# Performance work log

Hardware: AMD Instinct MI355X
Metric: run time of the kernel (lower is better)

Reference implementation:

```python
import jax, jax.numpy as jnp
import numpy as np
from jax import lax

B, T, D, U = 128, 1024, 256, 48


def setup_inputs() -> dict:
    key = jax.random.key(0)
    k1, k2, k3 = jax.random.split(key, 3)
    x = jax.random.normal(k1, (B, T, D), dtype=jnp.float32)
    kernel = jax.random.normal(k2, (D, U), dtype=jnp.float32) * (1.0 / np.sqrt(D))
    bias = jnp.zeros((U,), dtype=jnp.float32)
    chain_kernel = jax.random.normal(k3, (U, U), dtype=jnp.float32)
    return {"x": x, "kernel": kernel, "bias": bias, "chain_kernel": chain_kernel}


def _viterbi_decode(logits, trans):
    # logits: [B, T, U], trans: [U, U]; full-length sequences (mask=None)
    init_state = logits[:, 0]  # [B, U]
    steps = jnp.swapaxes(logits[:, 1:], 0, 1)  # [T-1, B, U]

    def fwd(state, logit_t):
        # scores[b, i, j] = state[b, i] + trans[i, j]
        scores = state[:, :, None] + trans[None]  # [B, U, U]
        bp = jnp.argmax(scores, axis=1)            # [B, U] best prev tag
        new_state = logit_t + jnp.max(scores, axis=1)
        return new_state, bp

    final_state, bps = lax.scan(fwd, init_state, steps)  # bps: [T-1, B, U]
    last_tag = jnp.argmax(final_state, axis=-1)          # [B]

    def back(tag, bp):
        prev = jnp.take_along_axis(bp, tag[:, None], axis=1)[:, 0]
        return prev, prev

    # reverse scan emits tags for t = 0..T-2 in forward time order
    _, tags_head = lax.scan(back, last_tag, bps, reverse=True)  # [T-1, B]
    tags = jnp.concatenate([tags_head, last_tag[None]], axis=0)  # [T, B]
    return jnp.transpose(tags)  # [B, T]


def reference(x, kernel, bias, chain_kernel):
    # _dense_layer: linear activation -> x @ kernel + bias
    logits = jnp.einsum('btd,du->btu', x, kernel) + bias  # [B, T, U]
    pred_ids = _viterbi_decode(logits, chain_kernel)       # [B, T] int
    return pred_ids.astype(jnp.float32)
```

## Files before the change

### kernel.cpp

```cpp
#include <hip/hip_runtime.h>
#include <cstdint>

#define B_ 128
#define T_ 1024
#define D_ 256
#define U_ 48

__global__ __launch_bounds__(256, 1) void k_logits(const float* __restrict__ x,
                                                   const float* __restrict__ kern,
                                                   const float* __restrict__ bias,
                                                   float* __restrict__ logits) {
    __shared__ float K[D_ * U_];
    __shared__ float bsh[U_];
    const int tid = threadIdx.x;
    for (int i = tid; i < D_ * U_; i += 256) K[i] = kern[i];
    if (tid < U_) bsh[tid] = bias[tid];
    __syncthreads();

    const long row0 = (long)blockIdx.x * 256 + tid;
    const long row1 = row0 + (long)B_ * T_ / 2;
    const float4* xr0 = (const float4*)(x + row0 * D_);
    const float4* xr1 = (const float4*)(x + row1 * D_);

    float a0[U_], a1[U_];
#pragma unroll
    for (int u = 0; u < U_; ++u) { a0[u] = 0.0f; a1[u] = 0.0f; }

#pragma unroll 1
    for (int d4 = 0; d4 < D_ / 4; ++d4) {
        const float4 xv0 = xr0[d4];
        const float4 xv1 = xr1[d4];
        const float xc0[4] = {xv0.x, xv0.y, xv0.z, xv0.w};
        const float xc1[4] = {xv1.x, xv1.y, xv1.z, xv1.w};
#pragma unroll
        for (int c = 0; c < 4; ++c) {
            const float4* kp = (const float4*)&K[(d4 * 4 + c) * U_];
            const float s0 = xc0[c], s1 = xc1[c];
#pragma unroll
            for (int u4 = 0; u4 < U_ / 4; ++u4) {
                float4 kv = kp[u4];
                a0[u4 * 4 + 0] += s0 * kv.x;  a1[u4 * 4 + 0] += s1 * kv.x;
                a0[u4 * 4 + 1] += s0 * kv.y;  a1[u4 * 4 + 1] += s1 * kv.y;
                a0[u4 * 4 + 2] += s0 * kv.z;  a1[u4 * 4 + 2] += s1 * kv.z;
                a0[u4 * 4 + 3] += s0 * kv.w;  a1[u4 * 4 + 3] += s1 * kv.w;
            }
        }
    }

    float4* o0 = (float4*)(logits + row0 * U_);
    float4* o1 = (float4*)(logits + row1 * U_);
#pragma unroll
    for (int i = 0; i < U_ / 4; ++i) {
        float4 v0, v1;
        v0.x = a0[i*4+0] + bsh[i*4+0];  v1.x = a1[i*4+0] + bsh[i*4+0];
        v0.y = a0[i*4+1] + bsh[i*4+1];  v1.y = a1[i*4+1] + bsh[i*4+1];
        v0.z = a0[i*4+2] + bsh[i*4+2];  v1.z = a1[i*4+2] + bsh[i*4+2];
        v0.w = a0[i*4+3] + bsh[i*4+3];  v1.w = a1[i*4+3] + bsh[i*4+3];
        o0[i] = v0;
        o1[i] = v1;
    }
}

__device__ __forceinline__ float step_max_lds(const float4* sb, const float* tc) {
    float n0 = -3.0e38f, n1 = -3.0e38f, n2 = -3.0e38f, n3 = -3.0e38f;
#pragma unroll
    for (int k = 0; k < U_ / 4; k += 4) {
        float4 s0 = sb[k + 0];
        float4 s1 = sb[k + 1];
        float4 s2 = sb[k + 2];
        float4 s3 = sb[k + 3];
        n0 = fmaxf(n0, fmaxf(fmaxf(s0.x + tc[4*k + 0],  s0.y + tc[4*k + 1]),
                             fmaxf(s0.z + tc[4*k + 2],  s0.w + tc[4*k + 3])));
        n1 = fmaxf(n1, fmaxf(fmaxf(s1.x + tc[4*k + 4],  s1.y + tc[4*k + 5]),
                             fmaxf(s1.z + tc[4*k + 6],  s1.w + tc[4*k + 7])));
        n2 = fmaxf(n2, fmaxf(fmaxf(s2.x + tc[4*k + 8],  s2.y + tc[4*k + 9]),
                             fmaxf(s2.z + tc[4*k + 10], s2.w + tc[4*k + 11])));
        n3 = fmaxf(n3, fmaxf(fmaxf(s3.x + tc[4*k + 12], s3.y + tc[4*k + 13]),
                             fmaxf(s3.z + tc[4*k + 14], s3.w + tc[4*k + 15])));
    }
    return fmaxf(fmaxf(n0, n1), fmaxf(n2, n3));
}

__global__ __launch_bounds__(64, 1) void k_forward(const float* __restrict__ trans,
                                                   const float* __restrict__ logits,
                                                   float* __restrict__ delta) {
    __shared__ float4 sbuf[2][U_ / 4];
    const int lane = threadIdx.x;
    const int b = blockIdx.x;
    const int u = (lane < U_) ? lane : (U_ - 1);

    float tc[U_];
#pragma unroll
    for (int v = 0; v < U_; ++v) tc[v] = trans[v * U_ + u];

    const float* lin = logits + (long)b * T_ * U_;
    float* dout = delta + (long)b * T_ * U_;

    float state = lin[u];
    dout[u] = state;
    ((float*)sbuf[0])[u] = state;

    float pf[8];
#pragma unroll
    for (int i = 0; i < 8; ++i) pf[i] = lin[(1 + i) * U_ + u];

    const float* lp = lin + 9 * U_ + u;
    float* dp = dout + 1 * U_ + u;

#pragma unroll 1
    for (int g = 0; g < 127; ++g) {
#pragma unroll
        for (int j = 0; j < 8; ++j) {
            const float logit = pf[j];
            pf[j] = lp[j * U_];

            const float4* sb = sbuf[j & 1];
            const float m = step_max_lds(sb, tc);
            state = logit + m;
            ((float*)sbuf[(j & 1) ^ 1])[u] = state;
            dp[j * U_] = state;
        }
        lp += 8 * U_;
        dp += 8 * U_;
    }

#pragma unroll
    for (int j = 0; j < 7; ++j) {
        const float logit = pf[j];
        const float4* sb = sbuf[j & 1];
        const float m = step_max_lds(sb, tc);
        state = logit + m;
        ((float*)sbuf[(j & 1) ^ 1])[u] = state;
        dp[j * U_] = state;
    }
}

__global__ __launch_bounds__(64, 1) void k_forward_inplace(const float* __restrict__ trans,
                                                           float* __restrict__ delta) {
    __shared__ float4 sbuf[2][U_ / 4];
    const int lane = threadIdx.x;
    const int b = blockIdx.x;
    const int u = (lane < U_) ? lane : (U_ - 1);

    float tc[U_];
#pragma unroll
    for (int v = 0; v < U_; ++v) tc[v] = trans[v * U_ + u];

    float* base = delta + (long)b * T_ * U_;
    float state = base[u];
    ((float*)sbuf[0])[u] = state;

#pragma unroll 1
    for (int t = 1; t < T_; ++t) {
        const float logit = base[(long)t * U_ + u];
        const float m = step_max_lds(sbuf[(t - 1) & 1], tc);
        state = logit + m;
        ((float*)sbuf[t & 1])[u] = state;
        base[(long)t * U_ + u] = state;
    }
}

__global__ __launch_bounds__(64, 1) void k_bp(const float* __restrict__ trans,
                                              const float* __restrict__ delta,
                                              unsigned char* __restrict__ bp) {
    const int lane = threadIdx.x;
    const int u = (lane < U_) ? lane : (U_ - 1);

    float tc[U_];
#pragma unroll
    for (int v = 0; v < U_; ++v) tc[v] = trans[v * U_ + u];

    const int NROW = B_ * (T_ - 1);
    const int stride = gridDim.x;

    int row = blockIdx.x;
    float dnext = 0.0f;
    if (row < NROW) {
        int b = row / (T_ - 1);
        int t = row - b * (T_ - 1) + 1;
        dnext = delta[((long)b * T_ + (t - 1)) * U_ + u];
    }
#pragma unroll 1
    for (; row < NROW; row += stride) {
        const float dv = dnext;
        const int rn = row + stride;
        if (rn < NROW) {
            int bn = rn / (T_ - 1);
            int tn = rn - bn * (T_ - 1) + 1;
            dnext = delta[((long)bn * T_ + (tn - 1)) * U_ + u];
        }
        const int db = __float_as_int(dv);
        float best = -3.4e38f;
        int bi = 0;
#pragma unroll
        for (int v = 0; v < U_; ++v) {
            float c = __int_as_float(__builtin_amdgcn_readlane(db, v)) + tc[v];
            if (c > best) { best = c; bi = v; }
        }
        if (lane < U_) bp[(long)row * U_ + u] = (unsigned char)bi;
    }
}

__global__ __launch_bounds__(64) void k_back(const float* __restrict__ delta,
                                             const unsigned char* __restrict__ bp,
                                             float* __restrict__ out) {
    __shared__ unsigned char bpl[(T_ - 1) * U_];
    __shared__ float tags[T_];
    __shared__ float fin[U_];
    const int lane = threadIdx.x;
    const int b = blockIdx.x;

    const uint32_t* src = (const uint32_t*)(bp + (long)b * (T_ - 1) * U_);
    uint32_t* dst = (uint32_t*)bpl;
    const int NW = (T_ - 1) * U_ / 4;
    for (int i = lane; i < NW; i += 64) dst[i] = src[i];
    if (lane < U_) fin[lane] = delta[((long)b * T_ + (T_ - 1)) * U_ + lane];
    __syncthreads();

    if (lane == 0) {
        float best = fin[0];
        int tag = 0;
        for (int uu = 1; uu < U_; ++uu)
            if (fin[uu] > best) { best = fin[uu]; tag = uu; }
        tags[T_ - 1] = (float)tag;
        for (int t = T_ - 1; t >= 1; --t) {
            tag = bpl[(t - 1) * U_ + tag];
            tags[t - 1] = (float)tag;
        }
    }
    __syncthreads();

    float* o = out + (long)b * T_;
    for (int i = lane; i < T_; i += 64) o[i] = tags[i];
}

extern "C" void kernel_launch(void* const* d_in, const int* in_sizes, int n_in,
                              void* d_out, int out_size, void* d_ws, size_t ws_size,
                              hipStream_t stream) {
    const float* x     = (const float*)d_in[0];
    const float* kern  = (const float*)d_in[1];
    const float* bias  = (const float*)d_in[2];
    const float* trans = (const float*)d_in[3];
    float* out = (float*)d_out;

    const size_t NBT = (size_t)B_ * T_ * U_ * sizeof(float);

    float* logits = (float*)d_ws;
    const bool two_buf = ws_size >= 2 * NBT + (size_t)B_ * T_ * U_;
    float* delta = two_buf ? (float*)((char*)d_ws + NBT) : logits;
    unsigned char* bp = (unsigned char*)d_ws + (two_buf ? 2 * NBT : NBT);

    k_logits<<<(B_ * T_ / 2) / 256, 256, 0, stream>>>(x, kern, bias, logits);
    if (two_buf)
        k_forward<<<B_, 64, 0, stream>>>(trans, logits, delta);
    else
        k_forward_inplace<<<B_, 64, 0, stream>>>(trans, logits);
    k_bp  <<<4096, 64, 0, stream>>>(trans, delta, bp);
    k_back<<<B_,   64, 0, stream>>>(delta, bp, out);
}
```

Measured before the change: 528.6 us.

## Batch x loads in logits GEMM, pack transition pairs, restructure backpointer kernel

The logits kernel now loads eight float4 of each x row per block before the FMA loop, which raises memory-level parallelism. The forward max step keeps transition coefficients as float2 pairs so the compiler can emit packed adds. The backpointer kernel now gives each block a contiguous run of 32 rows, broadcasts delta through LDS instead of readlane, and uses a branchless argmax. Lanes 48-63 now also write bp, duplicating lane 47's value to the same address, which is benign.

```diff
diff --git a/kernel.cpp b/kernel.cpp
--- a/kernel.cpp
+++ b/kernel.cpp
@@ -27,22 +27,30 @@
     for (int u = 0; u < U_; ++u) { a0[u] = 0.0f; a1[u] = 0.0f; }
 
 #pragma unroll 1
-    for (int d4 = 0; d4 < D_ / 4; ++d4) {
-        const float4 xv0 = xr0[d4];
-        const float4 xv1 = xr1[d4];
-        const float xc0[4] = {xv0.x, xv0.y, xv0.z, xv0.w};
-        const float xc1[4] = {xv1.x, xv1.y, xv1.z, xv1.w};
-#pragma unroll
-        for (int c = 0; c < 4; ++c) {
-            const float4* kp = (const float4*)&K[(d4 * 4 + c) * U_];
-            const float s0 = xc0[c], s1 = xc1[c];
-#pragma unroll
-            for (int u4 = 0; u4 < U_ / 4; ++u4) {
-                float4 kv = kp[u4];
-                a0[u4 * 4 + 0] += s0 * kv.x;  a1[u4 * 4 + 0] += s1 * kv.x;
-                a0[u4 * 4 + 1] += s0 * kv.y;  a1[u4 * 4 + 1] += s1 * kv.y;
-                a0[u4 * 4 + 2] += s0 * kv.z;  a1[u4 * 4 + 2] += s1 * kv.z;
-                a0[u4 * 4 + 3] += s0 * kv.w;  a1[u4 * 4 + 3] += s1 * kv.w;
+    for (int blk = 0; blk < D_ / 32; ++blk) {
+        float4 xa[8], xb[8];
+#pragma unroll
+        for (int i = 0; i < 8; ++i) xa[i] = xr0[blk * 8 + i];
+#pragma unroll
+        for (int i = 0; i < 8; ++i) xb[i] = xr1[blk * 8 + i];
+
+#pragma unroll
+        for (int i = 0; i < 8; ++i) {
+            const int d4 = blk * 8 + i;
+            const float xc0[4] = {xa[i].x, xa[i].y, xa[i].z, xa[i].w};
+            const float xc1[4] = {xb[i].x, xb[i].y, xb[i].z, xb[i].w};
+#pragma unroll
+            for (int c = 0; c < 4; ++c) {
+                const float4* kp = (const float4*)&K[(d4 * 4 + c) * U_];
+                const float s0 = xc0[c], s1 = xc1[c];
+#pragma unroll
+                for (int u4 = 0; u4 < U_ / 4; ++u4) {
+                    float4 kv = kp[u4];
+                    a0[u4*4+0] += s0 * kv.x;  a1[u4*4+0] += s1 * kv.x;
+                    a0[u4*4+1] += s0 * kv.y;  a1[u4*4+1] += s1 * kv.y;
+                    a0[u4*4+2] += s0 * kv.z;  a1[u4*4+2] += s1 * kv.z;
+                    a0[u4*4+3] += s0 * kv.w;  a1[u4*4+3] += s1 * kv.w;
+                }
             }
         }
     }
@@ -61,7 +69,7 @@
     }
 }
 
-__device__ __forceinline__ float step_max_lds(const float4* sb, const float* tc) {
+__device__ __forceinline__ float step_max_lds(const float4* sb, const float2* tc2) {
     float n0 = -3.0e38f, n1 = -3.0e38f, n2 = -3.0e38f, n3 = -3.0e38f;
 #pragma unroll
     for (int k = 0; k < U_ / 4; k += 4) {
@@ -69,14 +77,18 @@
         float4 s1 = sb[k + 1];
         float4 s2 = sb[k + 2];
         float4 s3 = sb[k + 3];
-        n0 = fmaxf(n0, fmaxf(fmaxf(s0.x + tc[4*k + 0],  s0.y + tc[4*k + 1]),
-                             fmaxf(s0.z + tc[4*k + 2],  s0.w + tc[4*k + 3])));
-        n1 = fmaxf(n1, fmaxf(fmaxf(s1.x + tc[4*k + 4],  s1.y + tc[4*k + 5]),
-                             fmaxf(s1.z + tc[4*k + 6],  s1.w + tc[4*k + 7])));
-        n2 = fmaxf(n2, fmaxf(fmaxf(s2.x + tc[4*k + 8],  s2.y + tc[4*k + 9]),
-                             fmaxf(s2.z + tc[4*k + 10], s2.w + tc[4*k + 11])));
-        n3 = fmaxf(n3, fmaxf(fmaxf(s3.x + tc[4*k + 12], s3.y + tc[4*k + 13]),
-                             fmaxf(s3.z + tc[4*k + 14], s3.w + tc[4*k + 15])));
+        float2 p0 = make_float2(s0.x + tc2[2*k+0].x, s0.y + tc2[2*k+0].y);
+        float2 p1 = make_float2(s0.z + tc2[2*k+1].x, s0.w + tc2[2*k+1].y);
+        float2 p2 = make_float2(s1.x + tc2[2*k+2].x, s1.y + tc2[2*k+2].y);
+        float2 p3 = make_float2(s1.z + tc2[2*k+3].x, s1.w + tc2[2*k+3].y);
+        float2 p4 = make_float2(s2.x + tc2[2*k+4].x, s2.y + tc2[2*k+4].y);
+        float2 p5 = make_float2(s2.z + tc2[2*k+5].x, s2.w + tc2[2*k+5].y);
+        float2 p6 = make_float2(s3.x + tc2[2*k+6].x, s3.y + tc2[2*k+6].y);
+        float2 p7 = make_float2(s3.z + tc2[2*k+7].x, s3.w + tc2[2*k+7].y);
+        n0 = fmaxf(n0, fmaxf(fmaxf(p0.x, p0.y), fmaxf(p1.x, p1.y)));
+        n1 = fmaxf(n1, fmaxf(fmaxf(p2.x, p2.y), fmaxf(p3.x, p3.y)));
+        n2 = fmaxf(n2, fmaxf(fmaxf(p4.x, p4.y), fmaxf(p5.x, p5.y)));
+        n3 = fmaxf(n3, fmaxf(fmaxf(p6.x, p6.y), fmaxf(p7.x, p7.y)));
     }
     return fmaxf(fmaxf(n0, n1), fmaxf(n2, n3));
 }
@@ -89,9 +101,12 @@
     const int b = blockIdx.x;
     const int u = (lane < U_) ? lane : (U_ - 1);
 
-    float tc[U_];
-#pragma unroll
-    for (int v = 0; v < U_; ++v) tc[v] = trans[v * U_ + u];
+    float2 tc2[U_ / 2];
+#pragma unroll
+    for (int v = 0; v < U_; v += 2) {
+        tc2[v / 2].x = trans[v * U_ + u];
+        tc2[v / 2].y = trans[(v + 1) * U_ + u];
+    }
 
     const float* lin = logits + (long)b * T_ * U_;
     float* dout = delta + (long)b * T_ * U_;
@@ -115,7 +130,7 @@
             pf[j] = lp[j * U_];
 
             const float4* sb = sbuf[j & 1];
-            const float m = step_max_lds(sb, tc);
+            const float m = step_max_lds(sb, tc2);
             state = logit + m;
             ((float*)sbuf[(j & 1) ^ 1])[u] = state;
             dp[j * U_] = state;
@@ -128,7 +143,7 @@
     for (int j = 0; j < 7; ++j) {
         const float logit = pf[j];
         const float4* sb = sbuf[j & 1];
-        const float m = step_max_lds(sb, tc);
+        const float m = step_max_lds(sb, tc2);
         state = logit + m;
         ((float*)sbuf[(j & 1) ^ 1])[u] = state;
         dp[j * U_] = state;
@@ -142,9 +157,12 @@
     const int b = blockIdx.x;
     const int u = (lane < U_) ? lane : (U_ - 1);
 
-    float tc[U_];
-#pragma unroll
-    for (int v = 0; v < U_; ++v) tc[v] = trans[v * U_ + u];
+    float2 tc2[U_ / 2];
+#pragma unroll
+    for (int v = 0; v < U_; v += 2) {
+        tc2[v / 2].x = trans[v * U_ + u];
+        tc2[v / 2].y = trans[(v + 1) * U_ + u];
+    }
 
     float* base = delta + (long)b * T_ * U_;
     float state = base[u];
@@ -153,16 +171,18 @@
 #pragma unroll 1
     for (int t = 1; t < T_; ++t) {
         const float logit = base[(long)t * U_ + u];
-        const float m = step_max_lds(sbuf[(t - 1) & 1], tc);
+        const float m = step_max_lds(sbuf[(t - 1) & 1], tc2);
         state = logit + m;
         ((float*)sbuf[t & 1])[u] = state;
         base[(long)t * U_ + u] = state;
     }
 }
 
+#define BP_ROWS 32
 __global__ __launch_bounds__(64, 1) void k_bp(const float* __restrict__ trans,
                                               const float* __restrict__ delta,
                                               unsigned char* __restrict__ bp) {
+    __shared__ float sbuf[2][U_];
     const int lane = threadIdx.x;
     const int u = (lane < U_) ? lane : (U_ - 1);
 
@@ -171,33 +191,44 @@
     for (int v = 0; v < U_; ++v) tc[v] = trans[v * U_ + u];
 
     const int NROW = B_ * (T_ - 1);
-    const int stride = gridDim.x;
-
-    int row = blockIdx.x;
-    float dnext = 0.0f;
-    if (row < NROW) {
-        int b = row / (T_ - 1);
-        int t = row - b * (T_ - 1) + 1;
-        dnext = delta[((long)b * T_ + (t - 1)) * U_ + u];
-    }
-#pragma unroll 1
-    for (; row < NROW; row += stride) {
-        const float dv = dnext;
-        const int rn = row + stride;
-        if (rn < NROW) {
-            int bn = rn / (T_ - 1);
-            int tn = rn - bn * (T_ - 1) + 1;
-            dnext = delta[((long)bn * T_ + (tn - 1)) * U_ + u];
-        }
-        const int db = __float_as_int(dv);
+    const int row0 = blockIdx.x * BP_ROWS;
+    if (row0 >= NROW) return;
+
+    int b = row0 / (T_ - 1);
+    int tm1 = row0 - b * (T_ - 1);
+
+    float dval = delta[((long)b * T_ + tm1) * U_ + u];
+
+#pragma unroll 1
+    for (int i = 0; i < BP_ROWS; ++i) {
+        const int row = row0 + i;
+        if (row >= NROW) break;
+
+        sbuf[i & 1][u] = dval;
+
+        int bn = b, tn = tm1 + 1;
+        if (tn == T_ - 1) { tn = 0; bn = b + 1; }
+        float dnext = 0.0f;
+        if (row + 1 < NROW) dnext = delta[((long)bn * T_ + tn) * U_ + u];
+
+        const float4* sb4 = (const float4*)sbuf[i & 1];
         float best = -3.4e38f;
         int bi = 0;
 #pragma unroll
-        for (int v = 0; v < U_; ++v) {
-            float c = __int_as_float(__builtin_amdgcn_readlane(db, v)) + tc[v];
-            if (c > best) { best = c; bi = v; }
-        }
-        if (lane < U_) bp[(long)row * U_ + u] = (unsigned char)bi;
+        for (int k = 0; k < U_ / 4; ++k) {
+            float4 s = sb4[k];
+            float c0 = s.x + tc[4*k+0];
+            float c1 = s.y + tc[4*k+1];
+            float c2 = s.z + tc[4*k+2];
+            float c3 = s.w + tc[4*k+3];
+            bi = (c0 > best) ? 4*k+0 : bi;  best = fmaxf(best, c0);
+            bi = (c1 > best) ? 4*k+1 : bi;  best = fmaxf(best, c1);
+            bi = (c2 > best) ? 4*k+2 : bi;  best = fmaxf(best, c2);
+            bi = (c3 > best) ? 4*k+3 : bi;  best = fmaxf(best, c3);
+        }
+        bp[(long)row * U_ + u] = (unsigned char)bi;
+
+        b = bn; tm1 = tn; dval = dnext;
     }
 }
 
@@ -250,11 +281,14 @@
     float* delta = two_buf ? (float*)((char*)d_ws + NBT) : logits;
     unsigned char* bp = (unsigned char*)d_ws + (two_buf ? 2 * NBT : NBT);
 
+    const int NROW = B_ * (T_ - 1);
+    const int bp_grid = (NROW + BP_ROWS - 1) / BP_ROWS;
+
     k_logits<<<(B_ * T_ / 2) / 256, 256, 0, stream>>>(x, kern, bias, logits);
     if (two_buf)
         k_forward<<<B_, 64, 0, stream>>>(trans, logits, delta);
     else
         k_forward_inplace<<<B_, 64, 0, stream>>>(trans, logits);
-    k_bp  <<<4096, 64, 0, stream>>>(trans, delta, bp);
-    k_back<<<B_,   64, 0, stream>>>(delta, bp, out);
-}
+    k_bp  <<<bp_grid, 64, 0, stream>>>(trans, delta, bp);
+    k_back<<<B_,      64, 0, stream>>>(delta, bp, out);
+}
```

New measurement: 515.7 us. 2.4% less time.
